# Kernel tuning notes

Hardware: AMD Instinct MI355X
Metric: run time of the kernel (lower is better)

The kernel has to match this reference:

```python
import jax, jax.numpy as jnp
import numpy as np

B, N, D, W = 4, 4096, 256, 7
K = 2 * W + 1  # 15 taps: positions [i-2w, ..., i]
H = 4 * D
EPS = 1e-5


def layer_norm(x, g, b):
    mu = jnp.mean(x, axis=-1, keepdims=True)
    var = jnp.mean(jnp.square(x - mu), axis=-1, keepdims=True)
    return (x - mu) * jax.lax.rsqrt(var + EPS) * g + b


def setup_inputs() -> dict:
    key = jax.random.key(0)
    ks = jax.random.split(key, 8)
    s = 0.02
    return {
        "x": jax.random.normal(ks[0], (B, N, D), dtype=jnp.float32),
        # w_mix[k] is the DxD block of the (K*D -> D) Linear acting on offset k-2w
        "w_mix": (jax.random.normal(ks[1], (K, D, D), dtype=jnp.float32) * s),
        "b_mix": jnp.zeros((D,), dtype=jnp.float32),
        "g1": jnp.ones((D,), jnp.float32) + 0.1 * jax.random.normal(ks[2], (D,), jnp.float32),
        "b1": 0.1 * jax.random.normal(ks[3], (D,), jnp.float32),
        "w_ff1": jax.random.normal(ks[4], (D, H), dtype=jnp.float32) * s,
        "b_ff1": jnp.zeros((H,), dtype=jnp.float32),
        "w_ff2": jax.random.normal(ks[5], (H, D), dtype=jnp.float32) * s,
        "b_ff2": jnp.zeros((D,), dtype=jnp.float32),
        "g2": jnp.ones((D,), jnp.float32) + 0.1 * jax.random.normal(ks[6], (D,), jnp.float32),
        "b2": 0.1 * jax.random.normal(ks[7], (D,), jnp.float32),
    }


def reference(x, w_mix, b_mix, g1, b1, w_ff1, b_ff1, w_ff2, b_ff2, g2, b2):
    # Causal windowed concat + Linear == causal 1D conv with kernel K=2w+1.
    # torch feats chunk k holds x[i - 2w + k]; conv tap k with left pad 2w
    # sees exactly x[i - 2w + k], so kernel = mix weight reshaped (K, D, D).
    mix = jax.lax.conv_general_dilated(
        x, w_mix, window_strides=(1,), padding=[(2 * W, 0)],
        dimension_numbers=("NWC", "WIO", "NWC"),
    ) + b_mix  # [B, N, D]
    # Dropout is identity in eval mode (reference baseline).
    h = layer_norm(x + mix, g1, b1)
    ff = jnp.dot(jax.nn.gelu(jnp.dot(h, w_ff1) + b_ff1, approximate=False), w_ff2) + b_ff2
    return layer_norm(h + ff, g2, b2)
```

## Files before the change

kernel.cpp:

```cpp
#include <hip/hip_runtime.h>
#include <cstdint>

#define DD     256
#define HH     1024
#define NNSEQ  4096
#define MT     32
#define XR     46
#define XPITCH 264
#define SLOTP  260
#define EPSLN  1e-5f

typedef unsigned short u16;
typedef __attribute__((ext_vector_type(8))) short short8;
typedef __attribute__((ext_vector_type(4))) float f32x4;

#define MFMA(a, b, c) __builtin_amdgcn_mfma_f32_16x16x32_bf16(a, b, c, 0, 0, 0)

__device__ __forceinline__ u16 f2bf(float f) {
  unsigned u = __float_as_uint(f);
  u += 0x7FFF + ((u >> 16) & 1);
  return (u16)(u >> 16);
}
__device__ __forceinline__ float bf2f(u16 s) { return __uint_as_float(((unsigned)s) << 16); }

__global__ __launch_bounds__(256) void k_prep(
    const float* __restrict__ wmix, const float* __restrict__ wff1,
    const float* __restrict__ wff2, u16* __restrict__ wpk,
    u16* __restrict__ w1pk, u16* __restrict__ w2pk)
{
  __shared__ float t[32][257];
  const int b = blockIdx.x, tid = threadIdx.x;

  u16* dst;
  if (b < 120) {
    dst = wpk + (size_t)b * 8192;
    for (int r = 0; r < 32; ++r)
      t[r][tid] = wmix[(size_t)(b * 32 + r) * 256 + tid];
  } else if (b < 152) {
    const int u = b - 120, c2 = u >> 3, s = u & 7;
    dst = w1pk + (size_t)u * 8192;
    for (int r = 0; r < 32; ++r)
      t[r][tid] = wff1[(size_t)(s * 32 + r) * 1024 + c2 * 256 + tid];
  } else {
    const int u = b - 152, c2 = u >> 3, s = u & 7;
    dst = w2pk + (size_t)u * 8192;
    for (int r = 0; r < 32; ++r)
      t[r][tid] = wff2[(size_t)(c2 * 256 + s * 32 + r) * 256 + tid];
  }
  __syncthreads();

  const int l = tid & 63, q = l >> 4, cl = l & 15;
#pragma unroll
  for (int f = 0; f < 4; ++f) {
    const int fi = f * 4 + (tid >> 6);
    const int n = fi * 16 + cl;
    uint4 pk;
    unsigned* p = (unsigned*)&pk;
#pragma unroll
    for (int jj = 0; jj < 4; ++jj)
      p[jj] = (unsigned)f2bf(t[q * 8 + jj * 2][n]) | ((unsigned)f2bf(t[q * 8 + jj * 2 + 1][n]) << 16);
    *(uint4*)&dst[(size_t)fi * 512 + l * 8] = pk;
  }
}

__global__ __launch_bounds__(512, 4) void k_fused(
    const float* __restrict__ x, const u16* __restrict__ wpk,
    const float* __restrict__ bmix, const float* __restrict__ g1,
    const float* __restrict__ b1, const u16* __restrict__ w1pk,
    const float* __restrict__ bf1, const u16* __restrict__ w2pk,
    const float* __restrict__ bf2, const float* __restrict__ g2,
    const float* __restrict__ b2, float* __restrict__ out)
{
  __shared__ u16 bufA[XR * XPITCH];
  __shared__ float bufB[MT * SLOTP];
  __shared__ float redS[8][MT], redS2[8][MT];
  __shared__ float muL[MT], invL[MT];

  const int tid = threadIdx.x;
  const int wv = tid >> 6, l = tid & 63, q = l >> 4, cl = l & 15;
  const int mg = wv >> 2, ng = wv & 3;
  const long tok0 = (long)blockIdx.x * MT;
  const int n0 = (int)(tok0 & (NNSEQ - 1));

  {
    const int cslot = (tid & 63) * 4;
    for (int r = tid >> 6; r < XR; r += 8) {
      const int nloc = n0 - 14 + r;
      float4 v = make_float4(0.f, 0.f, 0.f, 0.f);
      if (nloc >= 0) v = *(const float4*)&x[(tok0 - 14 + r) * DD + cslot];
      uint2 pk;
      pk.x = (unsigned)f2bf(v.x) | ((unsigned)f2bf(v.y) << 16);
      pk.y = (unsigned)f2bf(v.z) | ((unsigned)f2bf(v.w) << 16);
      *(uint2*)&bufA[r * XPITCH + cslot] = pk;
    }
  }
  __syncthreads();

  f32x4 acc[2][4];
#pragma unroll
  for (int nt = 0; nt < 4; ++nt) {
    const float bm = (mg == 0) ? bmix[ng * 64 + nt * 16 + cl] : 0.f;
#pragma unroll
    for (int mt = 0; mt < 2; ++mt) acc[mt][nt] = (f32x4){bm, bm, bm, bm};
  }

  const u16* bbase = wpk + (size_t)(mg * 60) * 8192 + (size_t)(ng * 4) * 512 + (size_t)l * 8;

#define LOAD_A(dst, s_)                                                         \
  {                                                                             \
    const int ks = mg * 60 + (s_);                                              \
    const int xrow = ks >> 3, c0 = (ks & 7) * 32;                               \
    _Pragma("unroll")                                                           \
    for (int mt = 0; mt < 2; ++mt)                                              \
      dst[mt] = *(const short8*)&bufA[(xrow + mt * 16 + cl) * XPITCH + c0 + q * 8]; \
  }
#define LOAD_B(dst, s_)                                                         \
  {                                                                             \
    const u16* bp = bbase + (size_t)(s_) * 8192;                                \
    _Pragma("unroll")                                                           \
    for (int nt = 0; nt < 4; ++nt)                                              \
      dst[nt] = *(const short8*)(bp + nt * 512);                                \
  }

  {
    short8 af[2][2], bfr[2][4];
    LOAD_A(af[0], 0) LOAD_B(bfr[0], 0)
    LOAD_A(af[1], 1) LOAD_B(bfr[1], 1)

#pragma unroll 2
    for (int s = 0; s < 60; ++s) {
      const int cur = s & 1;
#pragma unroll
      for (int mt = 0; mt < 2; ++mt)
#pragma unroll
        for (int nt = 0; nt < 4; ++nt)
          acc[mt][nt] = MFMA(af[cur][mt], bfr[cur][nt], acc[mt][nt]);
      if (s + 2 < 60) {
        LOAD_A(af[cur], s + 2)
        LOAD_B(bfr[cur], s + 2)
      }
    }
  }
#undef LOAD_A
#undef LOAD_B

  __syncthreads();
  if (mg == 1) {
#pragma unroll
    for (int mt = 0; mt < 2; ++mt)
#pragma unroll
      for (int nt = 0; nt < 4; ++nt)
#pragma unroll
        for (int reg = 0; reg < 4; ++reg)
          bufB[(mt * 16 + q * 4 + reg) * SLOTP + ng * 64 + nt * 16 + cl] = acc[mt][nt][reg];
  }
  __syncthreads();

  if (mg == 0) {
    float ps[2][4], ps2[2][4];
#pragma unroll
    for (int mt = 0; mt < 2; ++mt)
#pragma unroll
      for (int reg = 0; reg < 4; ++reg) {
        const int row = mt * 16 + q * 4 + reg;
        float s = 0.f, s2 = 0.f;
#pragma unroll
        for (int nt = 0; nt < 4; ++nt) {
          const int col = ng * 64 + nt * 16 + cl;
          const float y = acc[mt][nt][reg] + bufB[row * SLOTP + col]
                        + x[(tok0 + row) * DD + col];
          acc[mt][nt][reg] = y;
          s += y; s2 += y * y;
        }
#pragma unroll
        for (int off = 1; off < 16; off <<= 1) { s += __shfl_xor(s, off, 64); s2 += __shfl_xor(s2, off, 64); }
        ps[mt][reg] = s; ps2[mt][reg] = s2;
      }
    if (cl == 0) {
#pragma unroll
      for (int mt = 0; mt < 2; ++mt)
#pragma unroll
        for (int reg = 0; reg < 4; ++reg) {
          const int row = mt * 16 + q * 4 + reg;
          redS[ng][row] = ps[mt][reg]; redS2[ng][row] = ps2[mt][reg];
        }
    }
  }
  __syncthreads();
  if (tid < MT) {
    const float s  = redS[0][tid] + redS[1][tid] + redS[2][tid] + redS[3][tid];
    const float s2 = redS2[0][tid] + redS2[1][tid] + redS2[2][tid] + redS2[3][tid];
    const float mu = s * (1.f / DD);
    const float var = s2 * (1.f / DD) - mu * mu;
    muL[tid] = mu; invL[tid] = rsqrtf(var + EPSLN);
  }
  __syncthreads();

  if (mg == 0) {
#pragma unroll
    for (int nt = 0; nt < 4; ++nt) {
      const int col = ng * 64 + nt * 16 + cl;
      const float gv = g1[col], bv = b1[col];
#pragma unroll
      for (int mt = 0; mt < 2; ++mt)
#pragma unroll
        for (int reg = 0; reg < 4; ++reg) {
          const int row = mt * 16 + q * 4 + reg;
          const float hv = (acc[mt][nt][reg] - muL[row]) * invL[row] * gv + bv;
          bufA[row * XPITCH + col] = f2bf(hv);
        }
    }
  }
  __syncthreads();

  u16* asb = (u16*)bufB;
  f32x4 acc2[2][2];
#pragma unroll
  for (int nt = 0; nt < 2; ++nt) {
    const float bv = bf2[wv * 32 + nt * 16 + cl];
#pragma unroll
    for (int mt = 0; mt < 2; ++mt) acc2[mt][nt] = (f32x4){bv, bv, bv, bv};
  }

  for (int c = 0; c < 4; ++c) {
    f32x4 acc1[2][2];
#pragma unroll
    for (int nt = 0; nt < 2; ++nt) {
      const float bv = bf1[c * 256 + wv * 32 + nt * 16 + cl];
#pragma unroll
      for (int mt = 0; mt < 2; ++mt) acc1[mt][nt] = (f32x4){bv, bv, bv, bv};
    }
#pragma unroll
    for (int s = 0; s < 8; ++s) {
      short8 a[2], b[2];
#pragma unroll
      for (int mt = 0; mt < 2; ++mt)
        a[mt] = *(const short8*)&bufA[(mt * 16 + cl) * XPITCH + s * 32 + q * 8];
      const u16* bp = w1pk + (size_t)(c * 8 + s) * 8192 + (size_t)(wv * 2) * 512 + (size_t)l * 8;
#pragma unroll
      for (int nt = 0; nt < 2; ++nt)
        b[nt] = *(const short8*)(bp + nt * 512);
#pragma unroll
      for (int mt = 0; mt < 2; ++mt)
#pragma unroll
        for (int nt = 0; nt < 2; ++nt)
          acc1[mt][nt] = MFMA(a[mt], b[nt], acc1[mt][nt]);
    }
#pragma unroll
    for (int mt = 0; mt < 2; ++mt)
#pragma unroll
      for (int nt = 0; nt < 2; ++nt)
#pragma unroll
        for (int reg = 0; reg < 4; ++reg) {
          const float v = acc1[mt][nt][reg];
          const float g = 0.5f * v * (1.f + erff(v * 0.70710678118654752f));
          asb[(mt * 16 + q * 4 + reg) * XPITCH + wv * 32 + nt * 16 + cl] = f2bf(g);
        }
    __syncthreads();
#pragma unroll
    for (int s = 0; s < 8; ++s) {
      short8 a[2], b[2];
#pragma unroll
      for (int mt = 0; mt < 2; ++mt)
        a[mt] = *(const short8*)&asb[(mt * 16 + cl) * XPITCH + s * 32 + q * 8];
      const u16* bp = w2pk + (size_t)(c * 8 + s) * 8192 + (size_t)(wv * 2) * 512 + (size_t)l * 8;
#pragma unroll
      for (int nt = 0; nt < 2; ++nt)
        b[nt] = *(const short8*)(bp + nt * 512);
#pragma unroll
      for (int mt = 0; mt < 2; ++mt)
#pragma unroll
        for (int nt = 0; nt < 2; ++nt)
          acc2[mt][nt] = MFMA(a[mt], b[nt], acc2[mt][nt]);
    }
    __syncthreads();
  }

  {
    float ps[2][4], ps2[2][4];
#pragma unroll
    for (int mt = 0; mt < 2; ++mt)
#pragma unroll
      for (int reg = 0; reg < 4; ++reg) {
        const int row = mt * 16 + q * 4 + reg;
        float s = 0.f, s2 = 0.f;
#pragma unroll
        for (int nt = 0; nt < 2; ++nt) {
          const int col = wv * 32 + nt * 16 + cl;
          const float y = acc2[mt][nt][reg] + bf2f(bufA[row * XPITCH + col]);
          acc2[mt][nt][reg] = y;
          s += y; s2 += y * y;
        }
#pragma unroll
        for (int off = 1; off < 16; off <<= 1) { s += __shfl_xor(s, off, 64); s2 += __shfl_xor(s2, off, 64); }
        ps[mt][reg] = s; ps2[mt][reg] = s2;
      }
    if (cl == 0) {
#pragma unroll
      for (int mt = 0; mt < 2; ++mt)
#pragma unroll
        for (int reg = 0; reg < 4; ++reg) {
          const int row = mt * 16 + q * 4 + reg;
          redS[wv][row] = ps[mt][reg]; redS2[wv][row] = ps2[mt][reg];
        }
    }
  }
  __syncthreads();
  if (tid < MT) {
    float s = 0.f, s2 = 0.f;
#pragma unroll
    for (int k = 0; k < 8; ++k) { s += redS[k][tid]; s2 += redS2[k][tid]; }
    const float mu = s * (1.f / DD);
    const float var = s2 * (1.f / DD) - mu * mu;
    muL[tid] = mu; invL[tid] = rsqrtf(var + EPSLN);
  }
  __syncthreads();

#pragma unroll
  for (int nt = 0; nt < 2; ++nt) {
    const int col = wv * 32 + nt * 16 + cl;
    const float gv = g2[col], bv = b2[col];
#pragma unroll
    for (int mt = 0; mt < 2; ++mt)
#pragma unroll
      for (int reg = 0; reg < 4; ++reg) {
        const int row = mt * 16 + q * 4 + reg;
        out[(tok0 + row) * DD + col] = (acc2[mt][nt][reg] - muL[row]) * invL[row] * gv + bv;
      }
  }
}

extern "C" void kernel_launch(void* const* d_in, const int* in_sizes, int n_in,
                              void* d_out, int out_size, void* d_ws, size_t ws_size,
                              hipStream_t stream) {
  const float* x    = (const float*)d_in[0];
  const float* wmix = (const float*)d_in[1];
  const float* bmix = (const float*)d_in[2];
  const float* g1   = (const float*)d_in[3];
  const float* b1   = (const float*)d_in[4];
  const float* wff1 = (const float*)d_in[5];
  const float* bff1 = (const float*)d_in[6];
  const float* wff2 = (const float*)d_in[7];
  const float* bff2 = (const float*)d_in[8];
  const float* g2   = (const float*)d_in[9];
  const float* b2   = (const float*)d_in[10];
  float* out = (float*)d_out;

  u16* wpk  = (u16*)d_ws;
  u16* w1pk = wpk + 983040;
  u16* w2pk = w1pk + 262144;

  k_prep<<<184, 256, 0, stream>>>(wmix, wff1, wff2, wpk, w1pk, w2pk);

  k_fused<<<512, 512, 0, stream>>>(x, wpk, bmix, g1, b1,
                                   w1pk, bff1, w2pk, bff2, g2, b2, out);
}
```

Baseline: 157.6 us.

## Double token tile to 64 rows and drop split-K conv reduction

Each block now processes 64 tokens instead of 32, and all 8 waves split the output columns of the conv GEMM rather than splitting the K dimension into two halves that were reduced through shared memory. This halves weight traffic per token since each loaded B fragment feeds four M tiles, and removes the fp32 shared-memory reduction and its barriers. In exchange, register pressure rises, occupancy bound drops to 2 blocks per CU, the grid shrinks to 256 blocks (about one wave on the device), and the conv K loop is twice as long per wave, with a triple-buffered prefetch.

```diff
diff --git a/kernel.cpp b/kernel.cpp
--- a/kernel.cpp
+++ b/kernel.cpp
@@ -4,10 +4,9 @@
 #define DD     256
 #define HH     1024
 #define NNSEQ  4096
-#define MT     32
-#define XR     46
+#define MT     64
+#define XR     78
 #define XPITCH 264
-#define SLOTP  260
 #define EPSLN  1e-5f
 
 typedef unsigned short u16;
@@ -63,7 +62,7 @@
   }
 }
 
-__global__ __launch_bounds__(512, 4) void k_fused(
+__global__ __launch_bounds__(512, 2) void k_fused(
     const float* __restrict__ x, const u16* __restrict__ wpk,
     const float* __restrict__ bmix, const float* __restrict__ g1,
     const float* __restrict__ b1, const u16* __restrict__ w1pk,
@@ -72,19 +71,18 @@
     const float* __restrict__ b2, float* __restrict__ out)
 {
   __shared__ u16 bufA[XR * XPITCH];
-  __shared__ float bufB[MT * SLOTP];
+  __shared__ u16 asb[MT * XPITCH];
   __shared__ float redS[8][MT], redS2[8][MT];
   __shared__ float muL[MT], invL[MT];
 
   const int tid = threadIdx.x;
   const int wv = tid >> 6, l = tid & 63, q = l >> 4, cl = l & 15;
-  const int mg = wv >> 2, ng = wv & 3;
   const long tok0 = (long)blockIdx.x * MT;
   const int n0 = (int)(tok0 & (NNSEQ - 1));
 
   {
-    const int cslot = (tid & 63) * 4;
-    for (int r = tid >> 6; r < XR; r += 8) {
+    const int cslot = l * 4;
+    for (int r = wv; r < XR; r += 8) {
       const int nloc = n0 - 14 + r;
       float4 v = make_float4(0.f, 0.f, 0.f, 0.f);
       if (nloc >= 0) v = *(const float4*)&x[(tok0 - 14 + r) * DD + cslot];
@@ -96,79 +94,67 @@
   }
   __syncthreads();
 
-  f32x4 acc[2][4];
-#pragma unroll
-  for (int nt = 0; nt < 4; ++nt) {
-    const float bm = (mg == 0) ? bmix[ng * 64 + nt * 16 + cl] : 0.f;
-#pragma unroll
-    for (int mt = 0; mt < 2; ++mt) acc[mt][nt] = (f32x4){bm, bm, bm, bm};
-  }
-
-  const u16* bbase = wpk + (size_t)(mg * 60) * 8192 + (size_t)(ng * 4) * 512 + (size_t)l * 8;
+  f32x4 acc[4][2];
+#pragma unroll
+  for (int nt = 0; nt < 2; ++nt) {
+    const float bm = bmix[wv * 32 + nt * 16 + cl];
+#pragma unroll
+    for (int mt = 0; mt < 4; ++mt) acc[mt][nt] = (f32x4){bm, bm, bm, bm};
+  }
+
+  const u16* bbase = wpk + (size_t)(wv * 2) * 512 + (size_t)l * 8;
 
 #define LOAD_A(dst, s_)                                                         \
   {                                                                             \
-    const int ks = mg * 60 + (s_);                                              \
-    const int xrow = ks >> 3, c0 = (ks & 7) * 32;                               \
+    const int xrow = (s_) >> 3, c0 = ((s_) & 7) * 32;                           \
     _Pragma("unroll")                                                           \
-    for (int mt = 0; mt < 2; ++mt)                                              \
+    for (int mt = 0; mt < 4; ++mt)                                              \
       dst[mt] = *(const short8*)&bufA[(xrow + mt * 16 + cl) * XPITCH + c0 + q * 8]; \
   }
 #define LOAD_B(dst, s_)                                                         \
   {                                                                             \
     const u16* bp = bbase + (size_t)(s_) * 8192;                                \
     _Pragma("unroll")                                                           \
-    for (int nt = 0; nt < 4; ++nt)                                              \
+    for (int nt = 0; nt < 2; ++nt)                                              \
       dst[nt] = *(const short8*)(bp + nt * 512);                                \
   }
 
   {
-    short8 af[2][2], bfr[2][4];
+    short8 af[3][4], bfr[3][2];
     LOAD_A(af[0], 0) LOAD_B(bfr[0], 0)
     LOAD_A(af[1], 1) LOAD_B(bfr[1], 1)
-
-#pragma unroll 2
-    for (int s = 0; s < 60; ++s) {
-      const int cur = s & 1;
-#pragma unroll
-      for (int mt = 0; mt < 2; ++mt)
-#pragma unroll
-        for (int nt = 0; nt < 4; ++nt)
-          acc[mt][nt] = MFMA(af[cur][mt], bfr[cur][nt], acc[mt][nt]);
-      if (s + 2 < 60) {
-        LOAD_A(af[cur], s + 2)
-        LOAD_B(bfr[cur], s + 2)
+    LOAD_A(af[2], 2) LOAD_B(bfr[2], 2)
+
+    for (int sb = 0; sb < 120; sb += 3) {
+#pragma unroll
+      for (int u = 0; u < 3; ++u) {
+#pragma unroll
+        for (int mt = 0; mt < 4; ++mt)
+#pragma unroll
+          for (int nt = 0; nt < 2; ++nt)
+            acc[mt][nt] = MFMA(af[u][mt], bfr[u][nt], acc[mt][nt]);
+        if (sb + u + 3 < 120) {
+          LOAD_A(af[u], sb + u + 3)
+          LOAD_B(bfr[u], sb + u + 3)
+        }
       }
     }
   }
 #undef LOAD_A
 #undef LOAD_B
 
-  __syncthreads();
-  if (mg == 1) {
-#pragma unroll
-    for (int mt = 0; mt < 2; ++mt)
-#pragma unroll
-      for (int nt = 0; nt < 4; ++nt)
-#pragma unroll
-        for (int reg = 0; reg < 4; ++reg)
-          bufB[(mt * 16 + q * 4 + reg) * SLOTP + ng * 64 + nt * 16 + cl] = acc[mt][nt][reg];
-  }
-  __syncthreads();
-
-  if (mg == 0) {
-    float ps[2][4], ps2[2][4];
-#pragma unroll
-    for (int mt = 0; mt < 2; ++mt)
+  {
+    float ps[4][4], ps2[4][4];
+#pragma unroll
+    for (int mt = 0; mt < 4; ++mt)
 #pragma unroll
       for (int reg = 0; reg < 4; ++reg) {
         const int row = mt * 16 + q * 4 + reg;
         float s = 0.f, s2 = 0.f;
 #pragma unroll
-        for (int nt = 0; nt < 4; ++nt) {
-          const int col = ng * 64 + nt * 16 + cl;
-          const float y = acc[mt][nt][reg] + bufB[row * SLOTP + col]
-                        + x[(tok0 + row) * DD + col];
+        for (int nt = 0; nt < 2; ++nt) {
+          const int col = wv * 32 + nt * 16 + cl;
+          const float y = acc[mt][nt][reg] + x[(tok0 + row) * DD + col];
           acc[mt][nt][reg] = y;
           s += y; s2 += y * y;
         }
@@ -178,76 +164,74 @@
       }
     if (cl == 0) {
 #pragma unroll
-      for (int mt = 0; mt < 2; ++mt)
+      for (int mt = 0; mt < 4; ++mt)
 #pragma unroll
         for (int reg = 0; reg < 4; ++reg) {
           const int row = mt * 16 + q * 4 + reg;
-          redS[ng][row] = ps[mt][reg]; redS2[ng][row] = ps2[mt][reg];
+          redS[wv][row] = ps[mt][reg]; redS2[wv][row] = ps2[mt][reg];
         }
     }
   }
   __syncthreads();
   if (tid < MT) {
-    const float s  = redS[0][tid] + redS[1][tid] + redS[2][tid] + redS[3][tid];
-    const float s2 = redS2[0][tid] + redS2[1][tid] + redS2[2][tid] + redS2[3][tid];
+    float s = 0.f, s2 = 0.f;
+#pragma unroll
+    for (int k = 0; k < 8; ++k) { s += redS[k][tid]; s2 += redS2[k][tid]; }
     const float mu = s * (1.f / DD);
     const float var = s2 * (1.f / DD) - mu * mu;
     muL[tid] = mu; invL[tid] = rsqrtf(var + EPSLN);
   }
   __syncthreads();
 
-  if (mg == 0) {
-#pragma unroll
-    for (int nt = 0; nt < 4; ++nt) {
-      const int col = ng * 64 + nt * 16 + cl;
-      const float gv = g1[col], bv = b1[col];
-#pragma unroll
-      for (int mt = 0; mt < 2; ++mt)
-#pragma unroll
-        for (int reg = 0; reg < 4; ++reg) {
-          const int row = mt * 16 + q * 4 + reg;
-          const float hv = (acc[mt][nt][reg] - muL[row]) * invL[row] * gv + bv;
-          bufA[row * XPITCH + col] = f2bf(hv);
-        }
-    }
-  }
-  __syncthreads();
-
-  u16* asb = (u16*)bufB;
-  f32x4 acc2[2][2];
+#pragma unroll
+  for (int nt = 0; nt < 2; ++nt) {
+    const int col = wv * 32 + nt * 16 + cl;
+    const float gv = g1[col], bv = b1[col];
+#pragma unroll
+    for (int mt = 0; mt < 4; ++mt)
+#pragma unroll
+      for (int reg = 0; reg < 4; ++reg) {
+        const int row = mt * 16 + q * 4 + reg;
+        const float hv = (acc[mt][nt][reg] - muL[row]) * invL[row] * gv + bv;
+        bufA[row * XPITCH + col] = f2bf(hv);
+      }
+  }
+  __syncthreads();
+
+  f32x4 acc2[4][2];
 #pragma unroll
   for (int nt = 0; nt < 2; ++nt) {
     const float bv = bf2[wv * 32 + nt * 16 + cl];
 #pragma unroll
-    for (int mt = 0; mt < 2; ++mt) acc2[mt][nt] = (f32x4){bv, bv, bv, bv};
+    for (int mt = 0; mt < 4; ++mt) acc2[mt][nt] = (f32x4){bv, bv, bv, bv};
   }
 
   for (int c = 0; c < 4; ++c) {
-    f32x4 acc1[2][2];
+    f32x4 acc1[4][2];
 #pragma unroll
     for (int nt = 0; nt < 2; ++nt) {
       const float bv = bf1[c * 256 + wv * 32 + nt * 16 + cl];
 #pragma unroll
-      for (int mt = 0; mt < 2; ++mt) acc1[mt][nt] = (f32x4){bv, bv, bv, bv};
-    }
-#pragma unroll
+      for (int mt = 0; mt < 4; ++mt) acc1[mt][nt] = (f32x4){bv, bv, bv, bv};
+    }
+#pragma unroll 2
     for (int s = 0; s < 8; ++s) {
-      short8 a[2], b[2];
-#pragma unroll
-      for (int mt = 0; mt < 2; ++mt)
+      short8 a[4], b[2];
+#pragma unroll
+      for (int mt = 0; mt < 4; ++mt)
         a[mt] = *(const short8*)&bufA[(mt * 16 + cl) * XPITCH + s * 32 + q * 8];
       const u16* bp = w1pk + (size_t)(c * 8 + s) * 8192 + (size_t)(wv * 2) * 512 + (size_t)l * 8;
 #pragma unroll
       for (int nt = 0; nt < 2; ++nt)
         b[nt] = *(const short8*)(bp + nt * 512);
 #pragma unroll
-      for (int mt = 0; mt < 2; ++mt)
+      for (int mt = 0; mt < 4; ++mt)
 #pragma unroll
         for (int nt = 0; nt < 2; ++nt)
           acc1[mt][nt] = MFMA(a[mt], b[nt], acc1[mt][nt]);
     }
 #pragma unroll
-    for (int mt = 0; mt < 2; ++mt)
+    for (int mt = 0; mt < 4; ++mt)
 #pragma unroll
       for (int nt = 0; nt < 2; ++nt)
 #pragma unroll
@@ -257,18 +241,18 @@
           asb[(mt * 16 + q * 4 + reg) * XPITCH + wv * 32 + nt * 16 + cl] = f2bf(g);
         }
     __syncthreads();
-#pragma unroll
+#pragma unroll 2
     for (int s = 0; s < 8; ++s) {
-      short8 a[2], b[2];
-#pragma unroll
-      for (int mt = 0; mt < 2; ++mt)
+      short8 a[4], b[2];
+#pragma unroll
+      for (int mt = 0; mt < 4; ++mt)
         a[mt] = *(const short8*)&asb[(mt * 16 + cl) * XPITCH + s * 32 + q * 8];
       const u16* bp = w2pk + (size_t)(c * 8 + s) * 8192 + (size_t)(wv * 2) * 512 + (size_t)l * 8;
 #pragma unroll
       for (int nt = 0; nt < 2; ++nt)
         b[nt] = *(const short8*)(bp + nt * 512);
 #pragma unroll
-      for (int mt = 0; mt < 2; ++mt)
+      for (int mt = 0; mt < 4; ++mt)
 #pragma unroll
         for (int nt = 0; nt < 2; ++nt)
           acc2[mt][nt] = MFMA(a[mt], b[nt], acc2[mt][nt]);
@@ -277,9 +261,9 @@
   }
 
   {
-    float ps[2][4], ps2[2][4];
-#pragma unroll
-    for (int mt = 0; mt < 2; ++mt)
+    float ps[4][4], ps2[4][4];
+#pragma unroll
+    for (int mt = 0; mt < 4; ++mt)
 #pragma unroll
       for (int reg = 0; reg < 4; ++reg) {
         const int row = mt * 16 + q * 4 + reg;
@@ -297,7 +281,7 @@
       }
     if (cl == 0) {
 #pragma unroll
-      for (int mt = 0; mt < 2; ++mt)
+      for (int mt = 0; mt < 4; ++mt)
 #pragma unroll
         for (int reg = 0; reg < 4; ++reg) {
           const int row = mt * 16 + q * 4 + reg;
@@ -321,7 +305,7 @@
     const int col = wv * 32 + nt * 16 + cl;
     const float gv = g2[col], bv = b2[col];
 #pragma unroll
-    for (int mt = 0; mt < 2; ++mt)
+    for (int mt = 0; mt < 4; ++mt)
 #pragma unroll
       for (int reg = 0; reg < 4; ++reg) {
         const int row = mt * 16 + q * 4 + reg;
@@ -352,6 +336,6 @@
 
   k_prep<<<184, 256, 0, stream>>>(wmix, wff1, wff2, wpk, w1pk, w2pk);
 
-  k_fused<<<512, 512, 0, stream>>>(x, wpk, bmix, g1, b1,
+  k_fused<<<256, 512, 0, stream>>>(x, wpk, bmix, g1, b1,
                                    w1pk, bff1, w2pk, bff2, g2, b2, out);
 }
```

After: 162.0 us. 2.8% more time.
